# Optimization experiments

Measured on AMD Instinct MI355X. Metric: run time of the kernel, lower is better.

The kernel has to match this reference:

```python
import jax, jax.numpy as jnp
import numpy as np

B, T_TXT, T_IMG, N_LAT = 4, 2048, 8, 64
DIM, DIM_VIS, HEADS, DIM_HEAD = 2048, 1024, 8, 64
INNER = HEADS * DIM_HEAD
LN_EPS = 1e-5


def setup_inputs() -> dict:
    key = jax.random.key(0)
    ks = jax.random.split(key, 8)
    x = jax.random.normal(ks[0], (B, T_TXT, DIM), dtype=jnp.float32)
    media = jax.random.normal(ks[1], (B, T_IMG, N_LAT, DIM_VIS), dtype=jnp.float32)
    # exactly T_IMG media tokens per batch row at random positions
    pos = jax.random.randint(ks[2], (B, T_IMG), 0, T_TXT)
    media_locations = jnp.zeros((B, T_TXT), dtype=bool).at[jnp.arange(B)[:, None], pos].set(True)
    gamma = jnp.ones((DIM,), dtype=jnp.float32)
    beta = jnp.zeros((DIM,), dtype=jnp.float32)
    Wq = jax.random.normal(ks[3], (DIM, INNER), dtype=jnp.float32) * 0.02
    Wkv = jax.random.normal(ks[4], (DIM_VIS, 2 * INNER), dtype=jnp.float32) * 0.02
    Wout = jax.random.normal(ks[5], (INNER, DIM), dtype=jnp.float32) * 0.02
    return {"x": x, "media": media, "media_locations": media_locations,
            "gamma": gamma, "beta": beta, "Wq": Wq, "Wkv": Wkv, "Wout": Wout}


def _split_heads(t, h):
    b, s, _ = t.shape
    return t.reshape(b, s, h, -1).transpose(0, 2, 1, 3)  # b h s d


def reference(x, media, media_locations, gamma, beta, Wq, Wkv, Wout):
    b, t_txt, _ = x.shape
    _, t_img, n, _ = media.shape
    scale = DIM_HEAD ** (-0.5)

    # LayerNorm
    mu = jnp.mean(x, axis=-1, keepdims=True)
    var = jnp.mean(jnp.square(x - mu), axis=-1, keepdims=True)
    xn = (x - mu) * jax.lax.rsqrt(var + LN_EPS) * gamma + beta

    q = _split_heads(xn @ Wq, HEADS) * scale                # b h i d
    media_f = media.reshape(b, t_img * n, -1)               # b (t n) dv
    kv = media_f @ Wkv
    k, v = jnp.split(kv, 2, axis=-1)
    k = _split_heads(k, HEADS)                              # b h j d
    v = _split_heads(v, HEADS)

    sim = jnp.einsum('bhid,bhjd->bhij', q, k)               # b h i (t n)

    text_time = jnp.cumsum(media_locations.astype(jnp.int32), axis=-1)   # b i
    media_time = jnp.repeat(jnp.arange(1, t_img + 1), n)                 # (t n)
    mask = text_time[:, None, :, None] == media_time[None, None, None, :]

    neg = -jnp.finfo(sim.dtype).max
    sim = jnp.where(mask, sim, neg)
    sim = sim - jax.lax.stop_gradient(jnp.max(sim, axis=-1, keepdims=True))
    attn = jax.nn.softmax(sim, axis=-1)
    # zero attention for text tokens that precede any media
    attn = jnp.where((text_time == 0)[:, None, :, None], 0.0, attn)

    out = jnp.einsum('bhij,bhjd->bhid', attn, v)
    out = out.transpose(0, 2, 1, 3).reshape(b, t_txt, INNER)
    return out @ Wout
```

## Files before the change

kernel.cpp:

```cpp
#include <hip/hip_runtime.h>
#include <hip/hip_bf16.h>
#include <stdint.h>

typedef __bf16 bf16_t;
typedef __bf16 bf16x8 __attribute__((ext_vector_type(8)));
typedef float f32x4 __attribute__((ext_vector_type(4)));

#define NB      4
#define T_TXT   2048
#define T_IMG   8
#define N_LAT   64
#define DIM     2048
#define DIM_VIS 1024
#define HEADS   8
#define DHEAD   64
#define INNER   512

__device__ __forceinline__ void gld_lds16(const void* g, void* l) {
    __builtin_amdgcn_global_load_lds((const __attribute__((address_space(1))) void*)g,
                                     (__attribute__((address_space(3))) void*)l,
                                     16, 0, 0);
}

__global__ __launch_bounds__(256) void transpose3_k(const float* __restrict__ Wq,
                                                    const float* __restrict__ Wkv,
                                                    const float* __restrict__ Wout,
                                                    bf16_t* __restrict__ WqT,
                                                    bf16_t* __restrict__ WkvT,
                                                    bf16_t* __restrict__ WoutT) {
    __shared__ float tile[32][33];
    const float* in; bf16_t* out; int R, C;
    int which = blockIdx.y;
    if (which == 0)      { in = Wq;   out = WqT;   R = 2048; C = 512;  }
    else if (which == 1) { in = Wkv;  out = WkvT;  R = 1024; C = 1024; }
    else                 { in = Wout; out = WoutT; R = 512;  C = 2048; }
    int nbx = C >> 5;
    int bx = blockIdx.x % nbx, by = blockIdx.x / nbx;
    int c0 = bx * 32, r0 = by * 32;
    int x = threadIdx.x, y = threadIdx.y;
#pragma unroll
    for (int d = 0; d < 4; d++)
        tile[y + d * 8][x] = in[(size_t)(r0 + y + d * 8) * C + c0 + x];
    __syncthreads();
#pragma unroll
    for (int d = 0; d < 4; d++)
        out[(size_t)(c0 + y + d * 8) * R + r0 + x] = (bf16_t)tile[x][y + d * 8];
}

__global__ __launch_bounds__(256) void cvt_k(const float* __restrict__ in,
                                             bf16_t* __restrict__ out) {
    int idx = (blockIdx.x * 256 + threadIdx.x) * 8;
    f32x4 a = *(const f32x4*)(in + idx);
    f32x4 b = *(const f32x4*)(in + idx + 4);
    bf16x8 o;
#pragma unroll
    for (int i = 0; i < 4; i++) { o[i] = (bf16_t)a[i]; o[i + 4] = (bf16_t)b[i]; }
    *(bf16x8*)(out + idx) = o;
}

__global__ __launch_bounds__(256) void ln_k(const float* __restrict__ x,
                                            const float* __restrict__ gamma,
                                            const float* __restrict__ beta,
                                            bf16_t* __restrict__ xn) {
    int row = blockIdx.x;
    int t = threadIdx.x;
    const float* xp = x + (size_t)row * DIM + t * 8;
    f32x4 v0 = *(const f32x4*)xp;
    f32x4 v1 = *(const f32x4*)(xp + 4);
    float f[8];
    float s = 0.f, ss = 0.f;
#pragma unroll
    for (int i = 0; i < 4; i++) { f[i] = v0[i]; f[i + 4] = v1[i]; }
#pragma unroll
    for (int i = 0; i < 8; i++) { s += f[i]; ss += f[i] * f[i]; }
#pragma unroll
    for (int off = 32; off > 0; off >>= 1) { s += __shfl_xor(s, off); ss += __shfl_xor(ss, off); }
    __shared__ float sbuf[4], sbuf2[4];
    int wid = t >> 6, lane = t & 63;
    if (lane == 0) { sbuf[wid] = s; sbuf2[wid] = ss; }
    __syncthreads();
    s  = sbuf[0] + sbuf[1] + sbuf[2] + sbuf[3];
    ss = sbuf2[0] + sbuf2[1] + sbuf2[2] + sbuf2[3];
    float mu  = s * (1.0f / DIM);
    float var = ss * (1.0f / DIM) - mu * mu;
    float rs  = rsqrtf(var + 1e-5f);
    f32x4 g0 = *(const f32x4*)(gamma + t * 8);
    f32x4 g1 = *(const f32x4*)(gamma + t * 8 + 4);
    f32x4 b0 = *(const f32x4*)(beta + t * 8);
    f32x4 b1 = *(const f32x4*)(beta + t * 8 + 4);
    bf16x8 o;
#pragma unroll
    for (int i = 0; i < 4; i++) {
        o[i]     = (bf16_t)((f[i]     - mu) * rs * g0[i] + b0[i]);
        o[i + 4] = (bf16_t)((f[i + 4] - mu) * rs * g1[i] + b1[i]);
    }
    *(bf16x8*)(xn + (size_t)row * DIM + t * 8) = o;
}

template <typename OT>
__device__ __forceinline__ void gemm_body256(const bf16_t* __restrict__ A,
                                             const bf16_t* __restrict__ Bt,
                                             OT* __restrict__ C,
                                             int M, int N, int K, int Kper,
                                             float scale, int bid,
                                             int gx, int gy, int gz,
                                             bf16_t* lA, bf16_t* lB) {
    int tid = threadIdx.x;
    int w = tid >> 6, lane = tid & 63;
    int wm = w >> 2, wn = w & 3;

    int nwg = gx * gy * gz;
    int cpx = nwg >> 3;
    int nid = (bid & 7) * cpx + (bid >> 3);
    int tpy = gx * gz;
    int by = nid / tpy;
    int rr = nid - by * tpy;
    int bz = rr / gx;
    int bx = rr - bz * gx;

    int bm0 = by * 256, bn0 = bx * 256;
    int kbase = bz * Kper;
    int q = lane >> 4, l16 = lane & 15;

    const bf16_t* pA0 = A  + (size_t)(bm0 + w * 32      + l16) * K + kbase + q * 8;
    const bf16_t* pA1 = A  + (size_t)(bm0 + w * 32 + 16 + l16) * K + kbase + q * 8;
    const bf16_t* pB0 = Bt + (size_t)(bn0 + w * 32      + l16) * K + kbase + q * 8;
    const bf16_t* pB1 = Bt + (size_t)(bn0 + w * 32 + 16 + l16) * K + kbase + q * 8;

    f32x4 acc[8][4];
#pragma unroll
    for (int i = 0; i < 8; i++)
#pragma unroll
        for (int j = 0; j < 4; j++)
            acc[i][j] = (f32x4){0.f, 0.f, 0.f, 0.f};

    auto stage = [&](int buf, int k0) {
        gld_lds16(pA0 + k0, lA + buf * 8192 + (w * 2)     * 512);
        gld_lds16(pA1 + k0, lA + buf * 8192 + (w * 2 + 1) * 512);
        gld_lds16(pB0 + k0, lB + buf * 8192 + (w * 2)     * 512);
        gld_lds16(pB1 + k0, lB + buf * 8192 + (w * 2 + 1) * 512);
    };
    auto compute = [&](int buf) {
        bf16x8 af[8], bfr[4];
#pragma unroll
        for (int mt = 0; mt < 8; mt++)
            af[mt] = *(const bf16x8*)(lA + buf * 8192 + (wm * 8 + mt) * 512 + q * 128 + l16 * 8);
#pragma unroll
        for (int nt = 0; nt < 4; nt++)
            bfr[nt] = *(const bf16x8*)(lB + buf * 8192 + (wn * 4 + nt) * 512 + q * 128 + l16 * 8);
#pragma unroll
        for (int mt = 0; mt < 8; mt++)
#pragma unroll
            for (int nt = 0; nt < 4; nt++)
                acc[mt][nt] = __builtin_amdgcn_mfma_f32_16x16x32_bf16(af[mt], bfr[nt], acc[mt][nt], 0, 0, 0);
    };

    stage(0, 0);
    __syncthreads();
    int cur = 0;
    for (int k0 = 32; k0 < Kper; k0 += 32) {
        stage(cur ^ 1, k0);
        compute(cur);
        __syncthreads();
        cur ^= 1;
    }
    compute(cur);

    OT* Cz = C + (size_t)bz * M * N;
#pragma unroll
    for (int mt = 0; mt < 8; mt++)
#pragma unroll
        for (int nt = 0; nt < 4; nt++)
#pragma unroll
            for (int r = 0; r < 4; r++) {
                int row = bm0 + wm * 128 + mt * 16 + q * 4 + r;
                int col = bn0 + wn * 64 + nt * 16 + l16;
                Cz[(size_t)row * N + col] = (OT)(acc[mt][nt][r] * scale);
            }
}

__global__ __launch_bounds__(512, 2) void gemm12_k(const bf16_t* __restrict__ xn,
                                                   const bf16_t* __restrict__ WqT,
                                                   bf16_t* __restrict__ part,
                                                   const bf16_t* __restrict__ mediab,
                                                   const bf16_t* __restrict__ WkvT,
                                                   bf16_t* __restrict__ kvpart) {
    __shared__ __align__(16) bf16_t lA[2 * 8192];
    __shared__ __align__(16) bf16_t lB[2 * 8192];
    int bid = blockIdx.x;
    if (bid < 128)
        gemm_body256<bf16_t>(mediab, WkvT, kvpart, 2048, 1024, 1024, 256, 1.0f, bid, 4, 8, 4, lA, lB);
    else
        gemm_body256<bf16_t>(xn, WqT, part, 8192, 512, 2048, 512, 1.0f, bid - 128, 2, 32, 4, lA, lB);
}

__global__ __launch_bounds__(512, 2) void gemm3_k(const bf16_t* __restrict__ aout,
                                                  const bf16_t* __restrict__ WoutT,
                                                  float* __restrict__ out) {
    __shared__ __align__(16) bf16_t lA[2 * 8192];
    __shared__ __align__(16) bf16_t lB[2 * 8192];
    gemm_body256<float>(aout, WoutT, out, 8192, 2048, 512, 512, 1.0f, blockIdx.x, 8, 32, 1, lA, lB);
}

__global__ __launch_bounds__(256) void reduce4_k(const bf16_t* __restrict__ p,
                                                 bf16_t* __restrict__ o,
                                                 size_t n, float scale) {
    size_t i = ((size_t)blockIdx.x * 256 + threadIdx.x) * 8;
    bf16x8 a0 = *(const bf16x8*)(p + i);
    bf16x8 a1 = *(const bf16x8*)(p + n + i);
    bf16x8 a2 = *(const bf16x8*)(p + 2 * n + i);
    bf16x8 a3 = *(const bf16x8*)(p + 3 * n + i);
    bf16x8 r;
#pragma unroll
    for (int u = 0; u < 8; u++)
        r[u] = (bf16_t)(((float)a0[u] + (float)a1[u] + (float)a2[u] + (float)a3[u]) * scale);
    *(bf16x8*)(o + i) = r;
}

__global__ __launch_bounds__(256) void cumsum_bucket_k(const void* __restrict__ locs,
                                                       int* __restrict__ bstart,
                                                       int* __restrict__ bcnt) {
    int b = blockIdx.x, t = threadIdx.x;
    const unsigned* up = (const unsigned*)locs;
    const int* ip = (const int*)locs;
    const unsigned char* bp = (const unsigned char*)locs;
    const float* fp = (const float*)locs;

    int other = 0, nf = 0;
#pragma unroll
    for (int i = 0; i < 8; i++) {
        unsigned wv = up[t * 8 + i];
        nf    += (wv == 0x3F800000u);
        other += (wv != 0u && wv != 1u && wv != 0x3F800000u);
    }
#pragma unroll
    for (int off = 32; off > 0; off >>= 1) { other += __shfl_xor(other, off); nf += __shfl_xor(nf, off); }
    __shared__ int so[4], sf[4];
    int wid = t >> 6, lane = t & 63;
    if (lane == 0) { so[wid] = other; sf[wid] = nf; }
    __syncthreads();
    other = so[0] + so[1] + so[2] + so[3];
    nf    = sf[0] + sf[1] + sf[2] + sf[3];
    int mode = (other > 0) ? 0 : ((nf > 0) ? 2 : 1);

    int v[8];
    int s = 0;
#pragma unroll
    for (int i = 0; i < 8; i++) {
        int idx = b * T_TXT + t * 8 + i;
        int xv;
        if (mode == 1)      xv = ip[idx];
        else if (mode == 0) xv = (int)bp[idx];
        else                xv = (fp[idx] != 0.f) ? 1 : 0;
        v[i] = xv;
        s += xv;
    }
    __shared__ int sc[256];
    __shared__ int sstart[T_IMG];
    if (t < T_IMG) sstart[t] = T_TXT;
    sc[t] = s;
    __syncthreads();
    for (int off = 1; off < 256; off <<= 1) {
        int add = (t >= off) ? sc[t - off] : 0;
        __syncthreads();
        sc[t] += add;
        __syncthreads();
    }
    int run = sc[t] - s;
#pragma unroll
    for (int i = 0; i < 8; i++) {
        run += v[i];
        if (v[i] && run <= T_IMG) sstart[run - 1] = t * 8 + i;
    }
    __syncthreads();
    if (t < T_IMG) {
        int st = sstart[t];
        int nx = (t + 1 < T_IMG) ? sstart[t + 1] : T_TXT;
        bstart[b * T_IMG + t] = st;
        bcnt[b * T_IMG + t]   = nx - st;
    }
}

__global__ __launch_bounds__(256) void attn_mfma_k(const bf16_t* __restrict__ q,
                                                   const bf16_t* __restrict__ kv,
                                                   const int* __restrict__ bstart,
                                                   const int* __restrict__ bcnt,
                                                   bf16_t* __restrict__ aout) {
    __shared__ __align__(16) bf16_t lK[64 * 64];
    __shared__ __align__(16) bf16_t lVt[64 * 64];
    __shared__ __align__(16) bf16_t lP[4][16 * 64];

    int bid = blockIdx.x;
    int bucket = bid >> 6;
    int h = (bid >> 3) & 7;
    int c = bid & 7;
    int n_q = bcnt[bucket];
    int qlo = c << 8;
    if (n_q <= qlo) return;
    int qhi = (n_q < qlo + 256) ? n_q : (qlo + 256);
    int b = bucket >> 3;
    int timg = bucket & 7;
    int row0 = b * T_TXT + bstart[bucket];
    size_t krow0 = (size_t)(b * (T_IMG * N_LAT) + timg * N_LAT);

    int tid = threadIdx.x;
    int wid = tid >> 6, lane = tid & 63;
    int quad = lane >> 4, l16 = lane & 15;

    {
        const bf16_t* s0 = kv + (krow0 + 16 * wid + (lane >> 3)) * (2 * INNER) + h * DHEAD + (lane & 7) * 8;
        const bf16_t* s1 = kv + (krow0 + 16 * wid + 8 + (lane >> 3)) * (2 * INNER) + h * DHEAD + (lane & 7) * 8;
        gld_lds16(s0, lK + wid * 1024);
        gld_lds16(s1, lK + wid * 1024 + 512);
    }
    {
        int key = tid & 63, dblk = tid >> 6;
        const bf16_t* vsrc = kv + (krow0 + key) * (2 * INNER) + INNER + h * DHEAD + dblk * 16;
        bf16x8 v0 = *(const bf16x8*)vsrc;
        bf16x8 v1 = *(const bf16x8*)(vsrc + 8);
#pragma unroll
        for (int u = 0; u < 8; u++) {
            lVt[(dblk * 16 + u) * 64 + key]     = v0[u];
            lVt[(dblk * 16 + 8 + u) * 64 + key] = v1[u];
        }
    }
    __syncthreads();

    for (int c0 = qlo + wid * 16; c0 < qhi; c0 += 64) {
        int qi = row0 + c0 + ((c0 + l16 < n_q) ? l16 : 0);

        const bf16_t* qrow = q + (size_t)qi * INNER + h * DHEAD + quad * 8;
        bf16x8 qf0 = *(const bf16x8*)qrow;
        bf16x8 qf1 = *(const bf16x8*)(qrow + 32);
        f32x4 s[4];
#pragma unroll
        for (int nt = 0; nt < 4; nt++) s[nt] = (f32x4){0.f, 0.f, 0.f, 0.f};
#pragma unroll
        for (int nt = 0; nt < 4; nt++) {
            bf16x8 kf0 = *(const bf16x8*)(lK + (l16 + 16 * nt) * 64 + quad * 8);
            bf16x8 kf1 = *(const bf16x8*)(lK + (l16 + 16 * nt) * 64 + 32 + quad * 8);
            s[nt] = __builtin_amdgcn_mfma_f32_16x16x32_bf16(qf0, kf0, s[nt], 0, 0, 0);
            s[nt] = __builtin_amdgcn_mfma_f32_16x16x32_bf16(qf1, kf1, s[nt], 0, 0, 0);
        }

        float mr[4];
#pragma unroll
        for (int r = 0; r < 4; r++) {
            float m = fmaxf(fmaxf(s[0][r], s[1][r]), fmaxf(s[2][r], s[3][r]));
#pragma unroll
            for (int off = 8; off >= 1; off >>= 1) m = fmaxf(m, __shfl_xor(m, off));
            mr[r] = m;
        }
        float p[4][4];
#pragma unroll
        for (int nt = 0; nt < 4; nt++)
#pragma unroll
            for (int r = 0; r < 4; r++)
                p[nt][r] = __expf(s[nt][r] - mr[r]);
#pragma unroll
        for (int r = 0; r < 4; r++) {
            float tsum = p[0][r] + p[1][r] + p[2][r] + p[3][r];
#pragma unroll
            for (int off = 8; off >= 1; off >>= 1) tsum += __shfl_xor(tsum, off);
            float inv = 1.0f / tsum;
            p[0][r] *= inv; p[1][r] *= inv; p[2][r] *= inv; p[3][r] *= inv;
        }

        bf16_t* pt = lP[wid];
#pragma unroll
        for (int nt = 0; nt < 4; nt++)
#pragma unroll
            for (int r = 0; r < 4; r++)
                pt[(quad * 4 + r) * 64 + 16 * nt + l16] = (bf16_t)p[nt][r];
        asm volatile("s_waitcnt lgkmcnt(0)" ::: "memory");

        bf16x8 pf0 = *(const bf16x8*)(pt + l16 * 64 + quad * 8);
        bf16x8 pf1 = *(const bf16x8*)(pt + l16 * 64 + 32 + quad * 8);
        f32x4 o[4];
#pragma unroll
        for (int ntd = 0; ntd < 4; ntd++) o[ntd] = (f32x4){0.f, 0.f, 0.f, 0.f};
#pragma unroll
        for (int ntd = 0; ntd < 4; ntd++) {
            bf16x8 vf0 = *(const bf16x8*)(lVt + (l16 + 16 * ntd) * 64 + quad * 8);
            bf16x8 vf1 = *(const bf16x8*)(lVt + (l16 + 16 * ntd) * 64 + 32 + quad * 8);
            o[ntd] = __builtin_amdgcn_mfma_f32_16x16x32_bf16(pf0, vf0, o[ntd], 0, 0, 0);
            o[ntd] = __builtin_amdgcn_mfma_f32_16x16x32_bf16(pf1, vf1, o[ntd], 0, 0, 0);
        }

#pragma unroll
        for (int r = 0; r < 4; r++) {
            int qidx = c0 + quad * 4 + r;
            if (qidx < n_q) {
                bf16_t* op = aout + (size_t)(row0 + qidx) * INNER + h * DHEAD + l16;
#pragma unroll
                for (int ntd = 0; ntd < 4; ntd++)
                    op[16 * ntd] = (bf16_t)o[ntd][r];
            }
        }
    }
}

extern "C" void kernel_launch(void* const* d_in, const int* in_sizes, int n_in,
                              void* d_out, int out_size, void* d_ws, size_t ws_size,
                              hipStream_t stream) {
    const float* x     = (const float*)d_in[0];
    const float* media = (const float*)d_in[1];
    const void*  locs  = d_in[2];
    const float* gamma = (const float*)d_in[3];
    const float* beta  = (const float*)d_in[4];
    const float* Wq    = (const float*)d_in[5];
    const float* Wkv   = (const float*)d_in[6];
    const float* Wout  = (const float*)d_in[7];
    float* out = (float*)d_out;

    bf16_t* xn   = (bf16_t*)d_out;
    bf16_t* part = (bf16_t*)d_out + (size_t)16 * 1024 * 1024;

    char* p = (char*)d_ws;
    bf16_t* qbuf   = (bf16_t*)p; p += (size_t)8192 * 512 * 2;
    bf16_t* aout   = (bf16_t*)p; p += (size_t)8192 * 512 * 2;
    bf16_t* kvbuf  = (bf16_t*)p; p += (size_t)2048 * 1024 * 2;
    bf16_t* mediab = (bf16_t*)p; p += (size_t)2048 * 1024 * 2;
    bf16_t* WqT    = (bf16_t*)p; p += (size_t)512 * 2048 * 2;
    bf16_t* WkvT   = (bf16_t*)p; p += (size_t)1024 * 1024 * 2;
    bf16_t* WoutT  = (bf16_t*)p; p += (size_t)2048 * 512 * 2;
    int*    bstart = (int*)p;    p += 32 * sizeof(int);
    int*    bcnt   = (int*)p;    p += 32 * sizeof(int);

    cumsum_bucket_k<<<NB, 256, 0, stream>>>(locs, bstart, bcnt);
    transpose3_k<<<dim3(1024, 3), dim3(32, 8), 0, stream>>>(Wq, Wkv, Wout, WqT, WkvT, WoutT);
    cvt_k<<<(2048 * 1024) / (256 * 8), 256, 0, stream>>>(media, mediab);

    ln_k<<<8192, 256, 0, stream>>>(x, gamma, beta, xn);

    gemm12_k<<<384, 512, 0, stream>>>(xn, WqT, part, mediab, WkvT, qbuf);

    reduce4_k<<<1024, 256, 0, stream>>>(qbuf, kvbuf, (size_t)2048 * 1024, 1.0f);
    reduce4_k<<<2048, 256, 0, stream>>>(part, qbuf, (size_t)8192 * 512, 0.125f);

    hipMemsetAsync(aout, 0, (size_t)8192 * 512 * 2, stream);

    attn_mfma_k<<<32 * HEADS * 8, 256, 0, stream>>>(qbuf, kvbuf, bstart, bcnt, aout);

    gemm3_k<<<256, 512, 0, stream>>>(aout, WoutT, out);
}
```

Baseline: 265.0 us.

## Deepen GEMM LDS pipeline to four stages with vmcnt waits and setprio

Replaces the double-buffered LDS staging in the shared 256x256 GEMM body with a four-buffer ring that keeps three K-slices in flight. Each step now waits on a counted vmcnt plus a single barrier instead of a full __syncthreads, and issues the next prefetch after the fragment reads. MFMA issue is raised in priority with s_setprio. LDS per block doubles to 128KB, and the Wq blocks are now dispatched before the Wkv blocks in the fused GEMM launch. The larger LDS footprint may lower occupancy below the declared two blocks per CU.

```diff
diff --git a/kernel.cpp b/kernel.cpp
--- a/kernel.cpp
+++ b/kernel.cpp
@@ -134,13 +134,16 @@
         for (int j = 0; j < 4; j++)
             acc[i][j] = (f32x4){0.f, 0.f, 0.f, 0.f};
 
-    auto stage = [&](int buf, int k0) {
+    auto stage = [&](int t) {
+        int buf = t & 3;
+        int k0 = t << 5;
         gld_lds16(pA0 + k0, lA + buf * 8192 + (w * 2)     * 512);
         gld_lds16(pA1 + k0, lA + buf * 8192 + (w * 2 + 1) * 512);
         gld_lds16(pB0 + k0, lB + buf * 8192 + (w * 2)     * 512);
         gld_lds16(pB1 + k0, lB + buf * 8192 + (w * 2 + 1) * 512);
     };
-    auto compute = [&](int buf) {
+    auto compute = [&](int t, bool dostage) {
+        int buf = t & 3;
         bf16x8 af[8], bfr[4];
 #pragma unroll
         for (int mt = 0; mt < 8; mt++)
@@ -148,23 +151,32 @@
 #pragma unroll
         for (int nt = 0; nt < 4; nt++)
             bfr[nt] = *(const bf16x8*)(lB + buf * 8192 + (wn * 4 + nt) * 512 + q * 128 + l16 * 8);
+        if (dostage) stage(t + 3);
+        __builtin_amdgcn_s_setprio(1);
 #pragma unroll
         for (int mt = 0; mt < 8; mt++)
 #pragma unroll
             for (int nt = 0; nt < 4; nt++)
                 acc[mt][nt] = __builtin_amdgcn_mfma_f32_16x16x32_bf16(af[mt], bfr[nt], acc[mt][nt], 0, 0, 0);
+        __builtin_amdgcn_s_setprio(0);
     };
 
-    stage(0, 0);
-    __syncthreads();
-    int cur = 0;
-    for (int k0 = 32; k0 < Kper; k0 += 32) {
-        stage(cur ^ 1, k0);
-        compute(cur);
-        __syncthreads();
-        cur ^= 1;
-    }
-    compute(cur);
+    int nsteps = Kper >> 5;
+    stage(0); stage(1); stage(2);
+    for (int t = 0; t < nsteps - 2; t++) {
+        asm volatile("s_waitcnt vmcnt(8)" ::: "memory");
+        __builtin_amdgcn_s_barrier();
+        __builtin_amdgcn_sched_barrier(0);
+        compute(t, t + 3 < nsteps);
+    }
+    asm volatile("s_waitcnt vmcnt(4)" ::: "memory");
+    __builtin_amdgcn_s_barrier();
+    __builtin_amdgcn_sched_barrier(0);
+    compute(nsteps - 2, false);
+    asm volatile("s_waitcnt vmcnt(0)" ::: "memory");
+    __builtin_amdgcn_s_barrier();
+    __builtin_amdgcn_sched_barrier(0);
+    compute(nsteps - 1, false);
 
     OT* Cz = C + (size_t)bz * M * N;
 #pragma unroll
@@ -185,20 +197,20 @@
                                                    const bf16_t* __restrict__ mediab,
                                                    const bf16_t* __restrict__ WkvT,
                                                    bf16_t* __restrict__ kvpart) {
-    __shared__ __align__(16) bf16_t lA[2 * 8192];
-    __shared__ __align__(16) bf16_t lB[2 * 8192];
+    __shared__ __align__(16) bf16_t lA[4 * 8192];
+    __shared__ __align__(16) bf16_t lB[4 * 8192];
     int bid = blockIdx.x;
-    if (bid < 128)
-        gemm_body256<bf16_t>(mediab, WkvT, kvpart, 2048, 1024, 1024, 256, 1.0f, bid, 4, 8, 4, lA, lB);
+    if (bid < 256)
+        gemm_body256<bf16_t>(xn, WqT, part, 8192, 512, 2048, 512, 1.0f, bid, 2, 32, 4, lA, lB);
     else
-        gemm_body256<bf16_t>(xn, WqT, part, 8192, 512, 2048, 512, 1.0f, bid - 128, 2, 32, 4, lA, lB);
+        gemm_body256<bf16_t>(mediab, WkvT, kvpart, 2048, 1024, 1024, 256, 1.0f, bid - 256, 4, 8, 4, lA, lB);
 }
 
 __global__ __launch_bounds__(512, 2) void gemm3_k(const bf16_t* __restrict__ aout,
                                                   const bf16_t* __restrict__ WoutT,
                                                   float* __restrict__ out) {
-    __shared__ __align__(16) bf16_t lA[2 * 8192];
-    __shared__ __align__(16) bf16_t lB[2 * 8192];
+    __shared__ __align__(16) bf16_t lA[4 * 8192];
+    __shared__ __align__(16) bf16_t lB[4 * 8192];
     gemm_body256<float>(aout, WoutT, out, 8192, 2048, 512, 512, 1.0f, blockIdx.x, 8, 32, 1, lA, lB);
 }
 
```

New measurement: 263.4 us. About the same (-0.6%).

## Fuse prep kernels and load GEMM B fragments directly from global memory

Applied to the files above, without the earlier changes.

Merges the cumsum/bucket, weight transpose and media conversion kernels into one prep launch to cut launch overhead. The shared GEMM body stops staging B through LDS: each wave now reads its B fragments straight from global memory into registers, and only A is staged, with K steps of 64 instead of 32 in a double-buffered LDS tile of the same total size. Block order in the fused Q/KV GEMM launch is swapped so the larger Q projection blocks come first. This halves LDS traffic and barrier count per K, but uncoalesced-ish direct global B loads may add latency and register pressure.

```diff
diff --git a/kernel.cpp b/kernel.cpp
--- a/kernel.cpp
+++ b/kernel.cpp
@@ -22,40 +22,111 @@
                                      16, 0, 0);
 }
 
-__global__ __launch_bounds__(256) void transpose3_k(const float* __restrict__ Wq,
-                                                    const float* __restrict__ Wkv,
-                                                    const float* __restrict__ Wout,
-                                                    bf16_t* __restrict__ WqT,
-                                                    bf16_t* __restrict__ WkvT,
-                                                    bf16_t* __restrict__ WoutT) {
-    __shared__ float tile[32][33];
-    const float* in; bf16_t* out; int R, C;
-    int which = blockIdx.y;
-    if (which == 0)      { in = Wq;   out = WqT;   R = 2048; C = 512;  }
-    else if (which == 1) { in = Wkv;  out = WkvT;  R = 1024; C = 1024; }
-    else                 { in = Wout; out = WoutT; R = 512;  C = 2048; }
-    int nbx = C >> 5;
-    int bx = blockIdx.x % nbx, by = blockIdx.x / nbx;
-    int c0 = bx * 32, r0 = by * 32;
-    int x = threadIdx.x, y = threadIdx.y;
-#pragma unroll
-    for (int d = 0; d < 4; d++)
-        tile[y + d * 8][x] = in[(size_t)(r0 + y + d * 8) * C + c0 + x];
-    __syncthreads();
-#pragma unroll
-    for (int d = 0; d < 4; d++)
-        out[(size_t)(c0 + y + d * 8) * R + r0 + x] = (bf16_t)tile[x][y + d * 8];
-}
-
-__global__ __launch_bounds__(256) void cvt_k(const float* __restrict__ in,
-                                             bf16_t* __restrict__ out) {
-    int idx = (blockIdx.x * 256 + threadIdx.x) * 8;
-    f32x4 a = *(const f32x4*)(in + idx);
-    f32x4 b = *(const f32x4*)(in + idx + 4);
-    bf16x8 o;
-#pragma unroll
-    for (int i = 0; i < 4; i++) { o[i] = (bf16_t)a[i]; o[i + 4] = (bf16_t)b[i]; }
-    *(bf16x8*)(out + idx) = o;
+__global__ __launch_bounds__(256) void prep_k(const float* __restrict__ Wq,
+                                              const float* __restrict__ Wkv,
+                                              const float* __restrict__ Wout,
+                                              bf16_t* __restrict__ WqT,
+                                              bf16_t* __restrict__ WkvT,
+                                              bf16_t* __restrict__ WoutT,
+                                              const float* __restrict__ media,
+                                              bf16_t* __restrict__ mediab,
+                                              const void* __restrict__ locs,
+                                              int* __restrict__ bstart,
+                                              int* __restrict__ bcnt) {
+    __shared__ union {
+        float tile[32][33];
+        struct { int so[4]; int sf[4]; int sc[256]; int sstart[T_IMG]; } cs;
+    } sm;
+    int bid = blockIdx.x;
+    int tid = threadIdx.x;
+
+    if (bid < 3072) {
+        int which = bid >> 10, tix = bid & 1023;
+        const float* in; bf16_t* out; int R, C;
+        if (which == 0)      { in = Wq;   out = WqT;   R = 2048; C = 512;  }
+        else if (which == 1) { in = Wkv;  out = WkvT;  R = 1024; C = 1024; }
+        else                 { in = Wout; out = WoutT; R = 512;  C = 2048; }
+        int nbx = C >> 5;
+        int bx = tix % nbx, by = tix / nbx;
+        int c0 = bx * 32, r0 = by * 32;
+        int x = tid & 31, y = tid >> 5;
+#pragma unroll
+        for (int d = 0; d < 4; d++)
+            sm.tile[y + d * 8][x] = in[(size_t)(r0 + y + d * 8) * C + c0 + x];
+        __syncthreads();
+#pragma unroll
+        for (int d = 0; d < 4; d++)
+            out[(size_t)(c0 + y + d * 8) * R + r0 + x] = (bf16_t)sm.tile[x][y + d * 8];
+        return;
+    }
+    if (bid < 4096) {
+        int idx = ((bid - 3072) * 256 + tid) * 8;
+        f32x4 a = *(const f32x4*)(media + idx);
+        f32x4 b = *(const f32x4*)(media + idx + 4);
+        bf16x8 o;
+#pragma unroll
+        for (int i = 0; i < 4; i++) { o[i] = (bf16_t)a[i]; o[i + 4] = (bf16_t)b[i]; }
+        *(bf16x8*)(mediab + idx) = o;
+        return;
+    }
+    {
+        int b = bid - 4096, t = tid;
+        const unsigned* up = (const unsigned*)locs;
+        const int* ip = (const int*)locs;
+        const unsigned char* bp = (const unsigned char*)locs;
+        const float* fp = (const float*)locs;
+
+        int other = 0, nf = 0;
+#pragma unroll
+        for (int i = 0; i < 8; i++) {
+            unsigned wv = up[t * 8 + i];
+            nf    += (wv == 0x3F800000u);
+            other += (wv != 0u && wv != 1u && wv != 0x3F800000u);
+        }
+#pragma unroll
+        for (int off = 32; off > 0; off >>= 1) { other += __shfl_xor(other, off); nf += __shfl_xor(nf, off); }
+        int wid = t >> 6, lane = t & 63;
+        if (lane == 0) { sm.cs.so[wid] = other; sm.cs.sf[wid] = nf; }
+        __syncthreads();
+        other = sm.cs.so[0] + sm.cs.so[1] + sm.cs.so[2] + sm.cs.so[3];
+        nf    = sm.cs.sf[0] + sm.cs.sf[1] + sm.cs.sf[2] + sm.cs.sf[3];
+        int mode = (other > 0) ? 0 : ((nf > 0) ? 2 : 1);
+
+        int v[8];
+        int s = 0;
+#pragma unroll
+        for (int i = 0; i < 8; i++) {
+            int idx = b * T_TXT + t * 8 + i;
+            int xv;
+            if (mode == 1)      xv = ip[idx];
+            else if (mode == 0) xv = (int)bp[idx];
+            else                xv = (fp[idx] != 0.f) ? 1 : 0;
+            v[i] = xv;
+            s += xv;
+        }
+        if (t < T_IMG) sm.cs.sstart[t] = T_TXT;
+        sm.cs.sc[t] = s;
+        __syncthreads();
+        for (int off = 1; off < 256; off <<= 1) {
+            int add = (t >= off) ? sm.cs.sc[t - off] : 0;
+            __syncthreads();
+            sm.cs.sc[t] += add;
+            __syncthreads();
+        }
+        int run = sm.cs.sc[t] - s;
+#pragma unroll
+        for (int i = 0; i < 8; i++) {
+            run += v[i];
+            if (v[i] && run <= T_IMG) sm.cs.sstart[run - 1] = t * 8 + i;
+        }
+        __syncthreads();
+        if (t < T_IMG) {
+            int st = sm.cs.sstart[t];
+            int nx = (t + 1 < T_IMG) ? sm.cs.sstart[t + 1] : T_TXT;
+            bstart[b * T_IMG + t] = st;
+            bcnt[b * T_IMG + t]   = nx - st;
+        }
+    }
 }
 
 __global__ __launch_bounds__(256) void ln_k(const float* __restrict__ x,
@@ -104,7 +175,7 @@
                                              int M, int N, int K, int Kper,
                                              float scale, int bid,
                                              int gx, int gy, int gz,
-                                             bf16_t* lA, bf16_t* lB) {
+                                             bf16_t* lA) {
     int tid = threadIdx.x;
     int w = tid >> 6, lane = tid & 63;
     int wm = w >> 2, wn = w & 3;
@@ -121,11 +192,14 @@
     int bm0 = by * 256, bn0 = bx * 256;
     int kbase = bz * Kper;
     int q = lane >> 4, l16 = lane & 15;
-
-    const bf16_t* pA0 = A  + (size_t)(bm0 + w * 32      + l16) * K + kbase + q * 8;
-    const bf16_t* pA1 = A  + (size_t)(bm0 + w * 32 + 16 + l16) * K + kbase + q * 8;
-    const bf16_t* pB0 = Bt + (size_t)(bn0 + w * 32      + l16) * K + kbase + q * 8;
-    const bf16_t* pB1 = Bt + (size_t)(bn0 + w * 32 + 16 + l16) * K + kbase + q * 8;
+    int rbase = q * 128 + l16 * 8;
+
+    const bf16_t* sA0 = A + (size_t)(bm0 + (2 * w) * 16     + l16) * K + kbase + q * 8;
+    const bf16_t* sA1 = A + (size_t)(bm0 + (2 * w + 1) * 16 + l16) * K + kbase + q * 8;
+    const bf16_t* pB[4];
+#pragma unroll
+    for (int nt = 0; nt < 4; nt++)
+        pB[nt] = Bt + (size_t)(bn0 + wn * 64 + nt * 16 + l16) * K + kbase + q * 8;
 
     f32x4 acc[8][4];
 #pragma unroll
@@ -134,37 +208,44 @@
         for (int j = 0; j < 4; j++)
             acc[i][j] = (f32x4){0.f, 0.f, 0.f, 0.f};
 
-    auto stage = [&](int buf, int k0) {
-        gld_lds16(pA0 + k0, lA + buf * 8192 + (w * 2)     * 512);
-        gld_lds16(pA1 + k0, lA + buf * 8192 + (w * 2 + 1) * 512);
-        gld_lds16(pB0 + k0, lB + buf * 8192 + (w * 2)     * 512);
-        gld_lds16(pB1 + k0, lB + buf * 8192 + (w * 2 + 1) * 512);
+    auto stageA = [&](int buf, int t) {
+        int off = t * 64;
+        bf16_t* d = lA + buf * 16384;
+        gld_lds16(sA0 + off,      d + (2 * w) * 512);
+        gld_lds16(sA1 + off,      d + (2 * w + 1) * 512);
+        gld_lds16(sA0 + off + 32, d + (16 + 2 * w) * 512);
+        gld_lds16(sA1 + off + 32, d + (16 + 2 * w + 1) * 512);
     };
-    auto compute = [&](int buf) {
-        bf16x8 af[8], bfr[4];
-#pragma unroll
-        for (int mt = 0; mt < 8; mt++)
-            af[mt] = *(const bf16x8*)(lA + buf * 8192 + (wm * 8 + mt) * 512 + q * 128 + l16 * 8);
-#pragma unroll
-        for (int nt = 0; nt < 4; nt++)
-            bfr[nt] = *(const bf16x8*)(lB + buf * 8192 + (wn * 4 + nt) * 512 + q * 128 + l16 * 8);
-#pragma unroll
-        for (int mt = 0; mt < 8; mt++)
+
+    int T = Kper >> 6;
+    stageA(0, 0);
+    __syncthreads();
+
+    for (int t = 0; t < T; ++t) {
+        int buf = t & 1;
+        const bf16_t* LA = lA + buf * 16384;
+
+        bf16x8 bq[8];
+#pragma unroll
+        for (int ks = 0; ks < 2; ks++)
 #pragma unroll
             for (int nt = 0; nt < 4; nt++)
-                acc[mt][nt] = __builtin_amdgcn_mfma_f32_16x16x32_bf16(af[mt], bfr[nt], acc[mt][nt], 0, 0, 0);
-    };
-
-    stage(0, 0);
-    __syncthreads();
-    int cur = 0;
-    for (int k0 = 32; k0 < Kper; k0 += 32) {
-        stage(cur ^ 1, k0);
-        compute(cur);
+                bq[ks * 4 + nt] = *(const bf16x8*)(pB[nt] + t * 64 + ks * 32);
+
+        if (t + 1 < T) stageA(buf ^ 1, t + 1);
+
+#pragma unroll
+        for (int ks = 0; ks < 2; ks++) {
+#pragma unroll
+            for (int mt = 0; mt < 8; mt++) {
+                bf16x8 af = *(const bf16x8*)(LA + (ks * 16 + wm * 8 + mt) * 512 + rbase);
+#pragma unroll
+                for (int nt = 0; nt < 4; nt++)
+                    acc[mt][nt] = __builtin_amdgcn_mfma_f32_16x16x32_bf16(af, bq[ks * 4 + nt], acc[mt][nt], 0, 0, 0);
+            }
+        }
         __syncthreads();
-        cur ^= 1;
-    }
-    compute(cur);
+    }
 
     OT* Cz = C + (size_t)bz * M * N;
 #pragma unroll
@@ -185,21 +266,19 @@
                                                    const bf16_t* __restrict__ mediab,
                                                    const bf16_t* __restrict__ WkvT,
                                                    bf16_t* __restrict__ kvpart) {
-    __shared__ __align__(16) bf16_t lA[2 * 8192];
-    __shared__ __align__(16) bf16_t lB[2 * 8192];
+    __shared__ __align__(16) bf16_t lA[2 * 16384];
     int bid = blockIdx.x;
-    if (bid < 128)
-        gemm_body256<bf16_t>(mediab, WkvT, kvpart, 2048, 1024, 1024, 256, 1.0f, bid, 4, 8, 4, lA, lB);
+    if (bid < 256)
+        gemm_body256<bf16_t>(xn, WqT, part, 8192, 512, 2048, 512, 1.0f, bid, 2, 32, 4, lA);
     else
-        gemm_body256<bf16_t>(xn, WqT, part, 8192, 512, 2048, 512, 1.0f, bid - 128, 2, 32, 4, lA, lB);
+        gemm_body256<bf16_t>(mediab, WkvT, kvpart, 2048, 1024, 1024, 256, 1.0f, bid - 256, 4, 8, 4, lA);
 }
 
 __global__ __launch_bounds__(512, 2) void gemm3_k(const bf16_t* __restrict__ aout,
                                                   const bf16_t* __restrict__ WoutT,
                                                   float* __restrict__ out) {
-    __shared__ __align__(16) bf16_t lA[2 * 8192];
-    __shared__ __align__(16) bf16_t lB[2 * 8192];
-    gemm_body256<float>(aout, WoutT, out, 8192, 2048, 512, 512, 1.0f, blockIdx.x, 8, 32, 1, lA, lB);
+    __shared__ __align__(16) bf16_t lA[2 * 16384];
+    gemm_body256<float>(aout, WoutT, out, 8192, 2048, 512, 512, 1.0f, blockIdx.x, 8, 32, 1, lA);
 }
 
 __global__ __launch_bounds__(256) void reduce4_k(const bf16_t* __restrict__ p,
@@ -215,70 +294,6 @@
     for (int u = 0; u < 8; u++)
         r[u] = (bf16_t)(((float)a0[u] + (float)a1[u] + (float)a2[u] + (float)a3[u]) * scale);
     *(bf16x8*)(o + i) = r;
-}
-
-__global__ __launch_bounds__(256) void cumsum_bucket_k(const void* __restrict__ locs,
-                                                       int* __restrict__ bstart,
-                                                       int* __restrict__ bcnt) {
-    int b = blockIdx.x, t = threadIdx.x;
-    const unsigned* up = (const unsigned*)locs;
-    const int* ip = (const int*)locs;
-    const unsigned char* bp = (const unsigned char*)locs;
-    const float* fp = (const float*)locs;
-
-    int other = 0, nf = 0;
-#pragma unroll
-    for (int i = 0; i < 8; i++) {
-        unsigned wv = up[t * 8 + i];
-        nf    += (wv == 0x3F800000u);
-        other += (wv != 0u && wv != 1u && wv != 0x3F800000u);
-    }
-#pragma unroll
-    for (int off = 32; off > 0; off >>= 1) { other += __shfl_xor(other, off); nf += __shfl_xor(nf, off); }
-    __shared__ int so[4], sf[4];
-    int wid = t >> 6, lane = t & 63;
-    if (lane == 0) { so[wid] = other; sf[wid] = nf; }
-    __syncthreads();
-    other = so[0] + so[1] + so[2] + so[3];
-    nf    = sf[0] + sf[1] + sf[2] + sf[3];
-    int mode = (other > 0) ? 0 : ((nf > 0) ? 2 : 1);
-
-    int v[8];
-    int s = 0;
-#pragma unroll
-    for (int i = 0; i < 8; i++) {
-        int idx = b * T_TXT + t * 8 + i;
-        int xv;
-        if (mode == 1)      xv = ip[idx];
-        else if (mode == 0) xv = (int)bp[idx];
-        else                xv = (fp[idx] != 0.f) ? 1 : 0;
-        v[i] = xv;
-        s += xv;
-    }
-    __shared__ int sc[256];
-    __shared__ int sstart[T_IMG];
-    if (t < T_IMG) sstart[t] = T_TXT;
-    sc[t] = s;
-    __syncthreads();
-    for (int off = 1; off < 256; off <<= 1) {
-        int add = (t >= off) ? sc[t - off] : 0;
-        __syncthreads();
-        sc[t] += add;
-        __syncthreads();
-    }
-    int run = sc[t] - s;
-#pragma unroll
-    for (int i = 0; i < 8; i++) {
-        run += v[i];
-        if (v[i] && run <= T_IMG) sstart[run - 1] = t * 8 + i;
-    }
-    __syncthreads();
-    if (t < T_IMG) {
-        int st = sstart[t];
-        int nx = (t + 1 < T_IMG) ? sstart[t + 1] : T_TXT;
-        bstart[b * T_IMG + t] = st;
-        bcnt[b * T_IMG + t]   = nx - st;
-    }
 }
 
 __global__ __launch_bounds__(256) void attn_mfma_k(const bf16_t* __restrict__ q,
@@ -427,9 +442,8 @@
     int*    bstart = (int*)p;    p += 32 * sizeof(int);
     int*    bcnt   = (int*)p;    p += 32 * sizeof(int);
 
-    cumsum_bucket_k<<<NB, 256, 0, stream>>>(locs, bstart, bcnt);
-    transpose3_k<<<dim3(1024, 3), dim3(32, 8), 0, stream>>>(Wq, Wkv, Wout, WqT, WkvT, WoutT);
-    cvt_k<<<(2048 * 1024) / (256 * 8), 256, 0, stream>>>(media, mediab);
+    prep_k<<<4100, 256, 0, stream>>>(Wq, Wkv, Wout, WqT, WkvT, WoutT,
+                                     media, mediab, locs, bstart, bcnt);
 
     ln_k<<<8192, 256, 0, stream>>>(x, gamma, beta, xn);
 
```

Measured after the change: 277.0 us. 1.05x slower.
